# Optimization experiments

Measured on AMD Instinct MI355X. Metric: run time of the kernel, lower is better.

## Reference

```python
import jax, jax.numpy as jnp
import numpy as np

B, L, D = 8, 1024, 1024
H = 16
DPH = D // H  # 64
MAX_REL = 32  # relative position clip; vocab = 2*MAX_REL+1 (use_neg_dist=True)


def setup_inputs() -> dict:
    key = jax.random.key(0)
    ks = jax.random.split(key, 12)
    s = 1.0 / np.sqrt(D)
    return {
        "key": jax.random.normal(ks[0], (B, L, D), jnp.float32),
        "value": jax.random.normal(ks[1], (B, L, D), jnp.float32),
        "query": jax.random.normal(ks[2], (B, L, D), jnp.float32),
        "Wq": jax.random.normal(ks[3], (D, D), jnp.float32) * s,
        "bq": jnp.zeros((D,), jnp.float32),
        "Wk": jax.random.normal(ks[4], (D, D), jnp.float32) * s,
        "bk": jnp.zeros((D,), jnp.float32),
        "Wv": jax.random.normal(ks[5], (D, D), jnp.float32) * s,
        "bv": jnp.zeros((D,), jnp.float32),
        "Wo": jax.random.normal(ks[6], (D, D), jnp.float32) * s,
        "bo": jnp.zeros((D,), jnp.float32),
        "rel_emb": jax.random.normal(ks[7], (2 * MAX_REL + 1, DPH), jnp.float32) * 0.02,
    }


def reference(key, value, query, Wq, bq, Wk, bk, Wv, bv, Wo, bo, rel_emb):
    # shape: [B, L, D] -> [B, H, L, DPH]
    def shape(x):
        return x.reshape(B, L, H, DPH).transpose(0, 2, 1, 3)

    q = shape(query @ Wq.T + bq) / np.float32(np.sqrt(DPH))
    k = shape(key @ Wk.T + bk)
    v = shape(value @ Wv.T + bv)

    # relative position indices, clipped to [-MAX_REL, MAX_REL], shifted to [0, 2*MAX_REL]
    r = jnp.arange(L)
    dist = jnp.clip(r[None, :] - r[:, None], -MAX_REL, MAX_REL) + MAX_REL  # [L, L]
    rel = rel_emb[dist]  # [L, L, DPH]; same table for keys and values

    # scores = QK^T + Q . rel_keys  (relative_matmul with transpose=True)
    scores = jnp.einsum('bhqd,bhkd->bhqk', q, k) + jnp.einsum('bhqd,qkd->bhqk', q, rel)
    attn = jax.nn.softmax(scores.astype(jnp.float32), axis=-1).astype(q.dtype)

    # context = attn @ V + attn . rel_values (relative_matmul with transpose=False)
    ctx = jnp.einsum('bhqk,bhkd->bhqd', attn, v) + jnp.einsum('bhqk,qkd->bhqd', attn, rel)
    ctx = ctx.transpose(0, 2, 1, 3).reshape(B, L, D)
    out = ctx @ Wo.T + bo
    return out, attn
```

## Files before the change

kernel.cpp:

```cpp
#include <hip/hip_runtime.h>

typedef unsigned short u16;
typedef _Float16 f16;
typedef __attribute__((ext_vector_type(8))) _Float16 f16x8;
typedef __attribute__((ext_vector_type(4))) _Float16 f16x4;
typedef __attribute__((ext_vector_type(2))) _Float16 f16x2;
typedef __attribute__((ext_vector_type(4))) float f32x4;

#define MFMA16(acc, a, b) acc = __builtin_amdgcn_mfma_f32_16x16x32_f16(a, b, acc, 0, 0, 0)

__device__ __forceinline__ void gl2lds16(const void* g, void* l) {
  __builtin_amdgcn_global_load_lds(
      (const __attribute__((address_space(1))) void*)g,
      (__attribute__((address_space(3))) void*)l, 16, 0, 0);
}

__device__ __forceinline__ void cvt8(const float* __restrict__ src, f16* __restrict__ dst, int i) {
  const float* p = src + (size_t)i * 8;
  f32x4 a = *(const f32x4*)p;
  f32x4 b = *(const f32x4*)(p + 4);
  f16x8 o;
#pragma unroll
  for (int j = 0; j < 4; j++) {
    o[j] = (f16)a[j];
    o[j + 4] = (f16)b[j];
  }
  *(f16x8*)(dst + (size_t)i * 8) = o;
}

__global__ __launch_bounds__(256) void cvt_all(const float* __restrict__ Wq, const float* __restrict__ Wk,
                                               const float* __restrict__ Wv, const float* __restrict__ Wo,
                                               const float* __restrict__ rel, f16* __restrict__ f0,
                                               f16* __restrict__ f1, f16* __restrict__ f2,
                                               f16* __restrict__ f3, f16* __restrict__ fr) {
  const int NW = 131072;
  int i = blockIdx.x * 256 + threadIdx.x;
  if (i < NW) cvt8(Wq, f0, i);
  else if (i < 2 * NW) cvt8(Wk, f1, i - NW);
  else if (i < 3 * NW) cvt8(Wv, f2, i - 2 * NW);
  else if (i < 4 * NW) cvt8(Wo, f3, i - 3 * NW);
  else if (i < 4 * NW + 520) cvt8(rel, fr, i - 4 * NW);
}

__global__ __launch_bounds__(256) void gemm_qkv(const float* __restrict__ Aq, const float* __restrict__ Ak,
                                                const float* __restrict__ Av, const f16* __restrict__ W0,
                                                const f16* __restrict__ W1, const f16* __restrict__ W2,
                                                const float* __restrict__ b0, const float* __restrict__ b1,
                                                const float* __restrict__ b2, f16* __restrict__ O0,
                                                f16* __restrict__ O1, f16* __restrict__ O2) {
  int id = blockIdx.x;
  int which = id >> 9;
  int iid = id & 511;
  const float* A = (which == 0) ? Aq : (which == 1) ? Ak : Av;
  const f16* Wt = (which == 0) ? W0 : (which == 1) ? W1 : W2;
  const float* bias = (which == 0) ? b0 : (which == 1) ? b1 : b2;
  f16* out = (which == 0) ? O0 : (which == 1) ? O1 : O2;
  float scale = (which == 0) ? 0.125f : 1.0f;

  int m0 = (iid >> 3) << 7;
  int n0 = (iid & 7) << 7;
  int tid = threadIdx.x;
  int w = tid >> 6, lane = tid & 63, c = lane & 15, g = lane >> 4;
  int wm = (w >> 1) << 6, wn = (w & 1) << 6;

  __shared__ f16 As[128 * 32];
  __shared__ f16 Bs[128 * 32];

  f32x4 acc[4][4] = {};
  int ci0 = tid, ci1 = tid + 256;
  int r0 = ci0 >> 2, ks0 = (ci0 & 3) << 3;
  int r1 = ci1 >> 2, ks1 = (ci1 & 3) << 3;

  for (int k0 = 0; k0 < 1024; k0 += 32) {
    __syncthreads();
    gl2lds16(Wt + (size_t)(n0 + (ci0 >> 2)) * 1024 + k0 + ((ci0 & 3) << 3), Bs + w * 512);
    gl2lds16(Wt + (size_t)(n0 + (ci1 >> 2)) * 1024 + k0 + ((ci1 & 3) << 3), Bs + w * 512 + 2048);
    {
      const float* ap0 = A + (size_t)(m0 + r0) * 1024 + k0 + ks0;
      const float* ap1 = A + (size_t)(m0 + r1) * 1024 + k0 + ks1;
      f32x4 x0 = *(const f32x4*)ap0, x1 = *(const f32x4*)(ap0 + 4);
      f32x4 y0 = *(const f32x4*)ap1, y1 = *(const f32x4*)(ap1 + 4);
      f16x8 h0, h1;
#pragma unroll
      for (int j = 0; j < 4; j++) {
        h0[j] = (f16)x0[j];
        h0[j + 4] = (f16)x1[j];
        h1[j] = (f16)y0[j];
        h1[j + 4] = (f16)y1[j];
      }
      *(f16x8*)(As + (r0 << 5) + ks0) = h0;
      *(f16x8*)(As + (r1 << 5) + ks1) = h1;
    }
    __syncthreads();
    f16x8 af[4], bf[4];
#pragma unroll
    for (int mf = 0; mf < 4; mf++) af[mf] = *(const f16x8*)(As + ((wm + mf * 16 + c) << 5) + (g << 3));
#pragma unroll
    for (int nf = 0; nf < 4; nf++) bf[nf] = *(const f16x8*)(Bs + ((wn + nf * 16 + c) << 5) + (g << 3));
#pragma unroll
    for (int mf = 0; mf < 4; mf++)
#pragma unroll
      for (int nf = 0; nf < 4; nf++) MFMA16(acc[mf][nf], af[mf], bf[nf]);
  }

#pragma unroll
  for (int mf = 0; mf < 4; mf++)
#pragma unroll
    for (int nf = 0; nf < 4; nf++) {
      int row0 = m0 + wm + mf * 16 + (g << 2);
      int col = n0 + wn + nf * 16 + c;
      if (which == 2) {
        f16x4 vv;
#pragma unroll
        for (int r = 0; r < 4; r++) vv[r] = (f16)(acc[mf][nf][r] + bias[col]);
        size_t idx = (size_t)((row0 >> 10) * 16 + (col >> 6)) * 65536 + (size_t)(col & 63) * 1024 + (row0 & 1023);
        *(f16x4*)(out + idx) = vv;
      } else {
#pragma unroll
        for (int r = 0; r < 4; r++) {
          int row = row0 + r;
          size_t idx = (size_t)((row >> 10) * 16 + (col >> 6)) * 65536 + ((row & 1023) << 6) + (col & 63);
          out[idx] = (f16)((acc[mf][nf][r] + bias[col]) * scale);
        }
      }
    }
}

__global__ __launch_bounds__(256) void gemm_out(const f16* __restrict__ A, const f16* __restrict__ Wt,
                                                const float* __restrict__ bias, float* __restrict__ out) {
  int id = blockIdx.x;
  int m0 = (id >> 3) << 7;
  int n0 = (id & 7) << 7;
  int tid = threadIdx.x;
  int w = tid >> 6, lane = tid & 63, c = lane & 15, g = lane >> 4;
  int wm = (w >> 1) << 6, wn = (w & 1) << 6;

  __shared__ f16 As[128 * 32];
  __shared__ f16 Bs[128 * 32];

  f32x4 acc[4][4] = {};
  int ci0 = tid, ci1 = tid + 256;

  for (int k0 = 0; k0 < 1024; k0 += 32) {
    __syncthreads();
    gl2lds16(A + (size_t)(m0 + (ci0 >> 2)) * 1024 + k0 + ((ci0 & 3) << 3), As + w * 512);
    gl2lds16(A + (size_t)(m0 + (ci1 >> 2)) * 1024 + k0 + ((ci1 & 3) << 3), As + w * 512 + 2048);
    gl2lds16(Wt + (size_t)(n0 + (ci0 >> 2)) * 1024 + k0 + ((ci0 & 3) << 3), Bs + w * 512);
    gl2lds16(Wt + (size_t)(n0 + (ci1 >> 2)) * 1024 + k0 + ((ci1 & 3) << 3), Bs + w * 512 + 2048);
    __syncthreads();
    f16x8 af[4], bf[4];
#pragma unroll
    for (int mf = 0; mf < 4; mf++) af[mf] = *(const f16x8*)(As + ((wm + mf * 16 + c) << 5) + (g << 3));
#pragma unroll
    for (int nf = 0; nf < 4; nf++) bf[nf] = *(const f16x8*)(Bs + ((wn + nf * 16 + c) << 5) + (g << 3));
#pragma unroll
    for (int mf = 0; mf < 4; mf++)
#pragma unroll
      for (int nf = 0; nf < 4; nf++) MFMA16(acc[mf][nf], af[mf], bf[nf]);
  }

#pragma unroll
  for (int mf = 0; mf < 4; mf++)
#pragma unroll
    for (int nf = 0; nf < 4; nf++)
#pragma unroll
      for (int r = 0; r < 4; r++) {
        int row = m0 + wm + mf * 16 + (g << 2) + r;
        int col = n0 + wn + nf * 16 + c;
        out[(size_t)row * 1024 + col] = acc[mf][nf][r] + bias[col];
      }
}

__global__ __launch_bounds__(256) void attn_fused(const f16* __restrict__ Q, const f16* __restrict__ Km,
                                                  const f16* __restrict__ Vt, const f16* __restrict__ rel,
                                                  float* __restrict__ attn, f16* __restrict__ ctx) {
  int id = blockIdx.x;
  int sw = ((id & 7) << 10) + (id >> 3);
  int bh = sw >> 6;
  int q0 = (sw & 63) << 4;
  int b = bh >> 4, h = bh & 15;
  int tid = threadIdx.x;
  int w = tid >> 6, lane = tid & 63, c = lane & 15, g = lane >> 4;

  __shared__ float qrel_s[16 * 68];
  __shared__ float rmax[4][16], rsum[4][16], rlo[4][16], rhi[4][16];
  __shared__ float lo_s[16], hi_s[16];
  __shared__ f16 P_lds[1024 * 18];
  __shared__ f16 rel_s[65 * 64];

  const f16* Qb = Q + ((size_t)bh << 16);
  const f16* Kb = Km + ((size_t)bh << 16);
  const f16* Vtb = Vt + ((size_t)bh << 16);

  for (int i = tid; i < 65 * 64; i += 256) rel_s[i] = rel[i];

  f16x8 aq0 = *(const f16x8*)(Qb + ((q0 + c) << 6) + (g << 3));
  f16x8 aq1 = *(const f16x8*)(Qb + ((q0 + c) << 6) + 32 + (g << 3));

  if (w == 0) {
#pragma unroll
    for (int tf = 0; tf < 5; tf++) {
      int t = tf * 16 + c;
      int tc = (t < 65) ? t : 0;
      f32x4 ar = {};
      f16x8 b0 = *(const f16x8*)(rel + (tc << 6) + (g << 3));
      f16x8 b1 = *(const f16x8*)(rel + (tc << 6) + 32 + (g << 3));
      MFMA16(ar, aq0, b0);
      MFMA16(ar, aq1, b1);
      if (t < 65) {
#pragma unroll
        for (int r = 0; r < 4; r++) qrel_s[((g << 2) + r) * 68 + t] = ar[r];
      }
    }
  }
  __syncthreads();

  float s[16][4];
  int kbase = w << 8;
#pragma unroll
  for (int f = 0; f < 16; f++) {
    int kcol = kbase + (f << 4) + c;
    f32x4 a4 = {};
    f16x8 b0 = *(const f16x8*)(Kb + (kcol << 6) + (g << 3));
    f16x8 b1 = *(const f16x8*)(Kb + (kcol << 6) + 32 + (g << 3));
    MFMA16(a4, aq0, b0);
    MFMA16(a4, aq1, b1);
#pragma unroll
    for (int r = 0; r < 4; r++) {
      int rowl = (g << 2) + r;
      int d = kcol - (q0 + rowl);
      int t = (d < -32 ? -32 : (d > 32 ? 32 : d)) + 32;
      s[f][r] = a4[r] + qrel_s[rowl * 68 + t];
    }
  }

  float m[4] = {-3.0e38f, -3.0e38f, -3.0e38f, -3.0e38f};
#pragma unroll
  for (int f = 0; f < 16; f++)
#pragma unroll
    for (int r = 0; r < 4; r++) m[r] = fmaxf(m[r], s[f][r]);
#pragma unroll
  for (int mk = 1; mk <= 8; mk <<= 1)
#pragma unroll
    for (int r = 0; r < 4; r++) m[r] = fmaxf(m[r], __shfl_xor(m[r], mk, 64));
  if (c == 0) {
#pragma unroll
    for (int r = 0; r < 4; r++) rmax[w][(g << 2) + r] = m[r];
  }
  __syncthreads();
  float gm[4];
#pragma unroll
  for (int r = 0; r < 4; r++) {
    int rowl = (g << 2) + r;
    gm[r] = fmaxf(fmaxf(rmax[0][rowl], rmax[1][rowl]), fmaxf(rmax[2][rowl], rmax[3][rowl]));
  }
  float sum[4] = {0, 0, 0, 0}, lo[4] = {0, 0, 0, 0}, hi[4] = {0, 0, 0, 0};
#pragma unroll
  for (int f = 0; f < 16; f++)
#pragma unroll
    for (int r = 0; r < 4; r++) {
      float p = __expf(s[f][r] - gm[r]);
      s[f][r] = p;
      sum[r] += p;
      int d = (kbase + (f << 4) + c) - (q0 + (g << 2) + r);
      if (d <= -32) lo[r] += p;
      if (d >= 32) hi[r] += p;
    }
#pragma unroll
  for (int mk = 1; mk <= 8; mk <<= 1)
#pragma unroll
    for (int r = 0; r < 4; r++) {
      sum[r] += __shfl_xor(sum[r], mk, 64);
      lo[r] += __shfl_xor(lo[r], mk, 64);
      hi[r] += __shfl_xor(hi[r], mk, 64);
    }
  if (c == 0) {
#pragma unroll
    for (int r = 0; r < 4; r++) {
      int rowl = (g << 2) + r;
      rsum[w][rowl] = sum[r];
      rlo[w][rowl] = lo[r];
      rhi[w][rowl] = hi[r];
    }
  }
  __syncthreads();
  float inv[4];
#pragma unroll
  for (int r = 0; r < 4; r++) {
    int rowl = (g << 2) + r;
    float tot = rsum[0][rowl] + rsum[1][rowl] + rsum[2][rowl] + rsum[3][rowl];
    inv[r] = 1.0f / tot;
  }
  if (w == 0 && c == 0) {
#pragma unroll
    for (int r = 0; r < 4; r++) {
      int rowl = (g << 2) + r;
      float l4 = rlo[0][rowl] + rlo[1][rowl] + rlo[2][rowl] + rlo[3][rowl];
      float h4 = rhi[0][rowl] + rhi[1][rowl] + rhi[2][rowl] + rhi[3][rowl];
      lo_s[rowl] = l4 * inv[r];
      hi_s[rowl] = h4 * inv[r];
    }
  }

  float* ab = attn + ((size_t)bh << 20);
#pragma unroll
  for (int f = 0; f < 16; f++) {
    int k = kbase + (f << 4) + c;
    f16 ph[4];
#pragma unroll
    for (int r = 0; r < 4; r++) {
      float p = s[f][r] * inv[r];
      ab[((size_t)(q0 + (g << 2) + r) << 10) | (size_t)k] = p;
      ph[r] = (f16)p;
    }
    int koff = k * 18 + (g << 2);
    f16x2 p01 = {ph[0], ph[1]};
    f16x2 p23 = {ph[2], ph[3]};
    *(f16x2*)(P_lds + koff) = p01;
    *(f16x2*)(P_lds + koff + 2) = p23;
  }
  __syncthreads();

  f32x4 pv0 = {}, pv1 = {};
  const f16* vrow = Vtb + (size_t)((w << 4) + c) * 1024;
#pragma unroll 4
  for (int kk = 0; kk < 1024; kk += 64) {
    f16x8 aV0 = *(const f16x8*)(vrow + kk + (g << 3));
    f16x8 bP0;
#pragma unroll
    for (int j = 0; j < 8; j++) bP0[j] = P_lds[(kk + (g << 3) + j) * 18 + c];
    MFMA16(pv0, aV0, bP0);
    f16x8 aV1 = *(const f16x8*)(vrow + kk + 32 + (g << 3));
    f16x8 bP1;
#pragma unroll
    for (int j = 0; j < 8; j++) bP1[j] = P_lds[(kk + 32 + (g << 3) + j) * 18 + c];
    MFMA16(pv1, aV1, bP1);
  }

  int qg = q0 + c;
  float cval[4];
#pragma unroll
  for (int r = 0; r < 4; r++) {
    int d = (w << 4) + (g << 2) + r;
    cval[r] = pv0[r] + pv1[r] + lo_s[c] * (float)rel_s[d] + hi_s[c] * (float)rel_s[64 * 64 + d];
  }
  for (int t = 1; t < 64; t++) {
    int k = qg + t - 32;
    if (k >= 0 && k < 1024) {
      float pk = (float)P_lds[k * 18 + c];
#pragma unroll
      for (int r = 0; r < 4; r++) {
        int d = (w << 4) + (g << 2) + r;
        cval[r] += pk * (float)rel_s[t * 64 + d];
      }
    }
  }

#pragma unroll
  for (int r = 0; r < 4; r++) {
    int d = (w << 4) + (g << 2) + r;
    ctx[(((size_t)(b << 10) + qg) << 10) + (h << 6) + d] = (f16)cval[r];
  }
}

extern "C" void kernel_launch(void* const* d_in, const int* in_sizes, int n_in, void* d_out, int out_size,
                              void* d_ws, size_t ws_size, hipStream_t stream) {
  const float* key = (const float*)d_in[0];
  const float* value = (const float*)d_in[1];
  const float* query = (const float*)d_in[2];
  const float* Wq = (const float*)d_in[3];
  const float* bq = (const float*)d_in[4];
  const float* Wk = (const float*)d_in[5];
  const float* bk = (const float*)d_in[6];
  const float* Wv = (const float*)d_in[7];
  const float* bv = (const float*)d_in[8];
  const float* Wo = (const float*)d_in[9];
  const float* bo = (const float*)d_in[10];
  const float* rel = (const float*)d_in[11];

  char* ws = (char*)d_ws;
  f16* ctx = (f16*)(ws);
  f16* Wf0 = (f16*)(ws);
  f16* Wf1 = (f16*)(ws + (2u << 20));
  f16* Wf2 = (f16*)(ws + (4u << 20));
  f16* Qw = (f16*)(ws + (16u << 20));
  f16* Kw = (f16*)(ws + (32u << 20));
  f16* Vw = (f16*)(ws + (48u << 20));
  f16* Wf3 = (f16*)(ws + (64u << 20));
  f16* relf = (f16*)(ws + (66u << 20));

  float* outp = (float*)d_out;
  float* attnp = outp + (size_t)8 * 1024 * 1024;

  dim3 blk(256);
  cvt_all<<<2051, blk, 0, stream>>>(Wq, Wk, Wv, Wo, rel, Wf0, Wf1, Wf2, Wf3, relf);
  gemm_qkv<<<1536, blk, 0, stream>>>(query, key, value, Wf0, Wf1, Wf2, bq, bk, bv, Qw, Kw, Vw);
  attn_fused<<<8192, blk, 0, stream>>>(Qw, Kw, Vw, relf, attnp, ctx);
  gemm_out<<<512, blk, 0, stream>>>(ctx, Wf3, bo, outp);
}
```

Measured before the change: 499.1 us.

## Transpose P staging in LDS and write attention probabilities with coalesced stores

Stores the normalized probabilities in LDS as query-major rows with padding, then has all threads copy each row out to the attention output as contiguous 16-byte float4 stores. This replaces the earlier strided per-element global stores. The new layout also lets the PV MFMA B-operand and the relative-position loop read LDS with vector loads, and the rel table is read as f16x4. The attention output is now rounded through fp16 before being written as fp32, which lowers its precision.

After: 500.9 us. About the same (+0.4%).

```diff
diff --git a/kernel.cpp b/kernel.cpp
--- a/kernel.cpp
+++ b/kernel.cpp
@@ -185,7 +185,7 @@
   __shared__ float qrel_s[16 * 68];
   __shared__ float rmax[4][16], rsum[4][16], rlo[4][16], rhi[4][16];
   __shared__ float lo_s[16], hi_s[16];
-  __shared__ f16 P_lds[1024 * 18];
+  __shared__ f16 Pq[16][1032];
   __shared__ f16 rel_s[65 * 64];
 
   const f16* Qb = Q + ((size_t)bh << 16);
@@ -302,64 +302,62 @@
     }
   }
 
-  float* ab = attn + ((size_t)bh << 20);
 #pragma unroll
   for (int f = 0; f < 16; f++) {
     int k = kbase + (f << 4) + c;
-    f16 ph[4];
-#pragma unroll
-    for (int r = 0; r < 4; r++) {
-      float p = s[f][r] * inv[r];
-      ab[((size_t)(q0 + (g << 2) + r) << 10) | (size_t)k] = p;
-      ph[r] = (f16)p;
-    }
-    int koff = k * 18 + (g << 2);
-    f16x2 p01 = {ph[0], ph[1]};
-    f16x2 p23 = {ph[2], ph[3]};
-    *(f16x2*)(P_lds + koff) = p01;
-    *(f16x2*)(P_lds + koff + 2) = p23;
+#pragma unroll
+    for (int r = 0; r < 4; r++) Pq[(g << 2) + r][k] = (f16)(s[f][r] * inv[r]);
   }
   __syncthreads();
+
+  {
+    float* ab = attn + ((size_t)bh << 20) + ((size_t)q0 << 10);
+    int k4 = tid << 2;
+#pragma unroll
+    for (int ch = 0; ch < 16; ch++) {
+      f16x4 pv = *(const f16x4*)(&Pq[ch][k4]);
+      f32x4 o;
+#pragma unroll
+      for (int j = 0; j < 4; j++) o[j] = (float)pv[j];
+      *(f32x4*)(ab + ((size_t)ch << 10) + k4) = o;
+    }
+  }
 
   f32x4 pv0 = {}, pv1 = {};
   const f16* vrow = Vtb + (size_t)((w << 4) + c) * 1024;
 #pragma unroll 4
   for (int kk = 0; kk < 1024; kk += 64) {
     f16x8 aV0 = *(const f16x8*)(vrow + kk + (g << 3));
-    f16x8 bP0;
-#pragma unroll
-    for (int j = 0; j < 8; j++) bP0[j] = P_lds[(kk + (g << 3) + j) * 18 + c];
+    f16x8 bP0 = *(const f16x8*)(&Pq[c][kk + (g << 3)]);
     MFMA16(pv0, aV0, bP0);
     f16x8 aV1 = *(const f16x8*)(vrow + kk + 32 + (g << 3));
-    f16x8 bP1;
-#pragma unroll
-    for (int j = 0; j < 8; j++) bP1[j] = P_lds[(kk + 32 + (g << 3) + j) * 18 + c];
+    f16x8 bP1 = *(const f16x8*)(&Pq[c][kk + 32 + (g << 3)]);
     MFMA16(pv1, aV1, bP1);
   }
 
   int qg = q0 + c;
+  int d0 = (w << 4) + (g << 2);
   float cval[4];
-#pragma unroll
-  for (int r = 0; r < 4; r++) {
-    int d = (w << 4) + (g << 2) + r;
-    cval[r] = pv0[r] + pv1[r] + lo_s[c] * (float)rel_s[d] + hi_s[c] * (float)rel_s[64 * 64 + d];
+  {
+    f16x4 r0v = *(const f16x4*)(&rel_s[d0]);
+    f16x4 r64v = *(const f16x4*)(&rel_s[64 * 64 + d0]);
+#pragma unroll
+    for (int r = 0; r < 4; r++)
+      cval[r] = pv0[r] + pv1[r] + lo_s[c] * (float)r0v[r] + hi_s[c] * (float)r64v[r];
   }
   for (int t = 1; t < 64; t++) {
     int k = qg + t - 32;
     if (k >= 0 && k < 1024) {
-      float pk = (float)P_lds[k * 18 + c];
-#pragma unroll
-      for (int r = 0; r < 4; r++) {
-        int d = (w << 4) + (g << 2) + r;
-        cval[r] += pk * (float)rel_s[t * 64 + d];
-      }
+      float pk = (float)Pq[c][k];
+      f16x4 rv = *(const f16x4*)(&rel_s[t * 64 + d0]);
+#pragma unroll
+      for (int r = 0; r < 4; r++) cval[r] += pk * (float)rv[r];
     }
   }
 
 #pragma unroll
   for (int r = 0; r < 4; r++) {
-    int d = (w << 4) + (g << 2) + r;
-    ctx[(((size_t)(b << 10) + qg) << 10) + (h << 6) + d] = (f16)cval[r];
+    ctx[(((size_t)(b << 10) + qg) << 10) + (h << 6) + d0 + r] = (f16)cval[r];
   }
 }
 
```
